# Optimization experiments

Hardware: AMD Instinct MI355X
Metric: run time of the kernel (lower is better)

The kernel has to match this reference:

```python
import jax, jax.numpy as jnp
import numpy as np

B, S, D = 2, 2048, 512
H, DK, DV = 8, 64, 64
TEMP = DK ** 0.5


def setup_inputs() -> dict:
    key = jax.random.key(0)
    ks = jax.random.split(key, 12)
    inp = {
        "q": jax.random.normal(ks[0], (B, S, D), dtype=jnp.float32),
        "k": jax.random.normal(ks[1], (B, S, D), dtype=jnp.float32),
        "v": jax.random.normal(ks[2], (B, S, D), dtype=jnp.float32),
        "static_cov": jax.random.normal(ks[3], (B, S, S), dtype=jnp.float32),
        "mask": jax.random.randint(ks[4], (B, S, S), 0, 2, dtype=jnp.int32),
        # learned params (torch Linear(bias=False) weight is [out,in]; we store [in,out])
        "w_q": jax.random.normal(ks[5], (D, H * DK), dtype=jnp.float32) / np.sqrt(D),
        "w_k": jax.random.normal(ks[6], (D, H * DK), dtype=jnp.float32) / np.sqrt(D),
        "w_v": jax.random.normal(ks[7], (D, H * DV), dtype=jnp.float32) / np.sqrt(D),
        "w_fc": jax.random.normal(ks[8], (H * DV, D), dtype=jnp.float32) / np.sqrt(H * DV),
        "lambda_w": 10.0 * jnp.ones((1, H, 1, 1), dtype=jnp.float32),
        "ln_gamma": jnp.ones((D,), dtype=jnp.float32),
        "ln_beta": jnp.zeros((D,), dtype=jnp.float32),
    }
    return inp


def reference(q, k, v, static_cov, mask, w_q, w_k, w_v, w_fc, lambda_w, ln_gamma, ln_beta):
    residual = q
    # LayerNorm(eps=1e-6) on q only
    mu = jnp.mean(q, axis=-1, keepdims=True)
    var = jnp.mean(jnp.square(q - mu), axis=-1, keepdims=True)
    qn = (q - mu) / jnp.sqrt(var + 1e-6) * ln_gamma + ln_beta
    # projections -> [B, H, S, d]
    qh = (qn @ w_q).reshape(B, S, H, DK).transpose(0, 2, 1, 3)
    kh = (k @ w_k).reshape(B, S, H, DK).transpose(0, 2, 1, 3)
    vh = (v @ w_v).reshape(B, S, H, DV).transpose(0, 2, 1, 3)
    # convex blend of QK^T and static bias
    scores = jnp.einsum('bhqd,bhkd->bhqk', qh / TEMP, kh)  # [B,H,S,S]
    attn = scores / (lambda_w + 1.0) + (lambda_w / (lambda_w + 1.0)) * static_cov[:, None]
    attn = jnp.where(mask[:, None] == 0, -1e9, attn)
    attn = jax.nn.softmax(attn, axis=-1)
    out = jnp.einsum('bhqk,bhkd->bhqd', attn, vh)
    out = out.transpose(0, 2, 1, 3).reshape(B, S, H * DV)
    out = out @ w_fc + residual
    return (out, attn)
```

## Files before the change

kernel.cpp:

```cpp
#include <hip/hip_runtime.h>
#include <hip/hip_bf16.h>

typedef __attribute__((ext_vector_type(4))) float f32x4;
typedef __attribute__((ext_vector_type(4))) int i32x4;
typedef __attribute__((ext_vector_type(4))) unsigned int u32x4;
typedef __attribute__((ext_vector_type(8))) __bf16 bf16x8;
typedef __attribute__((ext_vector_type(4))) __bf16 bf16x4;

#define SDIM 2048
#define DDIM 512
#define HH 8
#define DH 64

static __device__ __forceinline__ f32x4 mfma_raw(bf16x8 a, bf16x8 b, f32x4 c) {
  return __builtin_amdgcn_mfma_f32_16x16x32_bf16(a, b, c, 0, 0, 0);
}

template <bool C1>
static __device__ __forceinline__ f32x4 mf(bf16x8 a, bf16x8 b, f32x4 c) {
  return C1 ? mfma_raw(a, b, c) : mfma_raw(b, a, c);
}

static __device__ __forceinline__ unsigned pack_bf16(float a, float b) {
  __bf16 x = (__bf16)a, y = (__bf16)b;
  unsigned short ux = __builtin_bit_cast(unsigned short, x);
  unsigned short uy = __builtin_bit_cast(unsigned short, y);
  return ((unsigned)uy << 16) | (unsigned)ux;
}

__global__ __launch_bounds__(256) void stageA_kernel(const float* __restrict__ cov,
                                                     const int* __restrict__ mask,
                                                     __bf16* __restrict__ covm,
                                                     const float* __restrict__ q,
                                                     const float* __restrict__ gamma,
                                                     const float* __restrict__ beta,
                                                     __bf16* __restrict__ qn,
                                                     const float* __restrict__ w0,
                                                     const float* __restrict__ w1,
                                                     const float* __restrict__ w2,
                                                     const float* __restrict__ w3,
                                                     __bf16* __restrict__ t0,
                                                     __bf16* __restrict__ t1,
                                                     __bf16* __restrict__ t2,
                                                     __bf16* __restrict__ t3,
                                                     int* __restrict__ flag) {
  __shared__ float tile[64][65];
  int bid = blockIdx.x;
  if (bid < 8192) {
    size_t i = ((size_t)bid * 256 + threadIdx.x) * 4;
    f32x4 c = *(const f32x4*)(cov + i);
    i32x4 m = *(const i32x4*)(mask + i);
    unsigned o = (unsigned)(i & 255);
    unsigned c16 = o >> 4;
    unsigned lgp = (o >> 2) & 3;
    size_t dst = (i & ~(size_t)255) + lgp * 64 + c16 * 4;
    bf16x4 ob;
#pragma unroll
    for (int r = 0; r < 4; ++r) ob[r] = (__bf16)((m[r] == 0) ? -1e38f : c[r]);
    *(bf16x4*)(covm + dst) = ob;
    return;
  }
  if (bid < 9216) {
    int lb = bid - 8192;
    if (lb == 0 && threadIdx.x < 64) {
      float av = (float)(threadIdx.x & 15);
      float bv = av * av;
      bf16x8 a, b;
#pragma unroll
      for (int i = 0; i < 8; ++i) { a[i] = (__bf16)av; b[i] = (__bf16)bv; }
      f32x4 d = {};
      d = mfma_raw(a, b, d);
      if (threadIdx.x == 17) *flag = (d[0] == 128.0f) ? 1 : 2;
    }
    int row = lb * 4 + (threadIdx.x >> 6);
    int lane = threadIdx.x & 63;
    const float* qr = q + (size_t)row * DDIM + lane * 8;
    f32x4 x0 = *(const f32x4*)qr;
    f32x4 x1 = *(const f32x4*)(qr + 4);
    float s = 0.f;
#pragma unroll
    for (int i = 0; i < 4; ++i) s += x0[i] + x1[i];
#pragma unroll
    for (int off = 32; off; off >>= 1) s += __shfl_xor(s, off);
    float mu = s * (1.f / DDIM);
    float vs = 0.f;
#pragma unroll
    for (int i = 0; i < 4; ++i) {
      float d0 = x0[i] - mu, d1 = x1[i] - mu;
      vs += d0 * d0 + d1 * d1;
    }
#pragma unroll
    for (int off = 32; off; off >>= 1) vs += __shfl_xor(vs, off);
    float inv = rsqrtf(vs * (1.f / DDIM) + 1e-6f);
    const float* g = gamma + lane * 8;
    const float* be = beta + lane * 8;
    bf16x8 o;
#pragma unroll
    for (int i = 0; i < 8; ++i) {
      float xv = (i < 4) ? x0[i] : x1[i - 4];
      o[i] = (__bf16)((xv - mu) * inv * g[i] + be[i]);
    }
    *(bf16x8*)(qn + (size_t)row * DDIM + lane * 8) = o;
    return;
  }
  int wb = bid - 9216;
  int which = wb >> 6;
  int rem = wb & 63;
  int n0 = (rem & 7) * 64;
  int k0 = (rem >> 3) * 64;
  const float* w = which == 0 ? w0 : which == 1 ? w1 : which == 2 ? w2 : w3;
  __bf16* t = which == 0 ? t0 : which == 1 ? t1 : which == 2 ? t2 : t3;
  int tx = threadIdx.x & 63, ty = threadIdx.x >> 6;
#pragma unroll
  for (int j = 0; j < 16; ++j) {
    int kk = ty * 16 + j;
    tile[kk][tx] = w[(size_t)(k0 + kk) * DDIM + n0 + tx];
  }
  __syncthreads();
#pragma unroll
  for (int j = 0; j < 16; ++j) {
    int n = ty * 16 + j;
    t[(size_t)(n0 + n) * DDIM + k0 + tx] = (__bf16)tile[tx][n];
  }
}

template <bool C1>
static __device__ __forceinline__ void proj_body(const __bf16* __restrict__ qn,
                                                 const float* __restrict__ kin,
                                                 const float* __restrict__ vin,
                                                 const __bf16* __restrict__ wqT,
                                                 const __bf16* __restrict__ wkT,
                                                 const __bf16* __restrict__ wvT,
                                                 const float* __restrict__ lam,
                                                 __bf16* __restrict__ qh,
                                                 __bf16* __restrict__ kh,
                                                 __bf16* __restrict__ vT,
                                                 __bf16* __restrict__ tr) {
  int which = blockIdx.z;
  int n0 = blockIdx.x * 64;
  int m0 = blockIdx.y * 64;
  int wid = threadIdx.x >> 6, lane = threadIdx.x & 63;
  int lr = lane & 15, lg = lane >> 4;
  int mrow = m0 + wid * 16;
  const __bf16* wT = which == 0 ? wqT : which == 1 ? wkT : wvT;
  f32x4 acc[4] = {};
  for (int kb = 0; kb < DDIM; kb += 32) {
    bf16x8 afrag;
    if (which == 0) {
      afrag = *(const bf16x8*)(qn + (size_t)(mrow + lr) * DDIM + kb + lg * 8);
    } else {
      const float* src = (which == 1 ? kin : vin) + (size_t)(mrow + lr) * DDIM + kb + lg * 8;
      f32x4 y0 = *(const f32x4*)src;
      f32x4 y1 = *(const f32x4*)(src + 4);
#pragma unroll
      for (int i = 0; i < 4; ++i) { afrag[i] = (__bf16)y0[i]; afrag[i + 4] = (__bf16)y1[i]; }
    }
#pragma unroll
    for (int c = 0; c < 4; ++c) {
      bf16x8 bfrag = *(const bf16x8*)(wT + (size_t)(n0 + c * 16 + lr) * DDIM + kb + lg * 8);
      acc[c] = mf<C1>(afrag, bfrag, acc[c]);
    }
  }
  int h = n0 >> 6;
  int bq = m0 >> 11;
  int ss0 = m0 & 2047;
  if (which == 0) {
    float sc = 1.f / (8.f * (lam[h] + 1.f));
#pragma unroll
    for (int c = 0; c < 4; ++c)
#pragma unroll
      for (int r = 0; r < 4; ++r)
        tr[(wid * 16 + lg * 4 + r) * 72 + c * 16 + lr] = (__bf16)(acc[c][r] * sc);
  } else if (which == 1) {
#pragma unroll
    for (int c = 0; c < 4; ++c)
#pragma unroll
      for (int r = 0; r < 4; ++r)
        tr[(wid * 16 + lg * 4 + r) * 72 + c * 16 + lr] = (__bf16)acc[c][r];
  } else {
#pragma unroll
    for (int c = 0; c < 4; ++c)
#pragma unroll
      for (int r = 0; r < 4; ++r)
        tr[(c * 16 + lr) * 72 + wid * 16 + lg * 4 + r] = (__bf16)acc[c][r];
  }
  __syncthreads();
  size_t bh2 = (size_t)bq * HH + h;
#pragma unroll
  for (int ii = 0; ii < 2; ++ii) {
    int row = (threadIdx.x >> 3) + ii * 32;
    int col = (threadIdx.x & 7) * 8;
    bf16x8 v8 = *(const bf16x8*)(tr + row * 72 + col);
    if (which == 2) {
      *(bf16x8*)(vT + (bh2 * DH + row) * SDIM + ss0 + col) = v8;
    } else {
      __bf16* dst = (which == 0 ? qh : kh);
      *(bf16x8*)(dst + (bh2 * SDIM + ss0 + row) * DH + col) = v8;
    }
  }
}

__global__ __launch_bounds__(256) void proj_kernel(const __bf16* __restrict__ qn,
                                                   const float* __restrict__ kin,
                                                   const float* __restrict__ vin,
                                                   const __bf16* __restrict__ wqT,
                                                   const __bf16* __restrict__ wkT,
                                                   const __bf16* __restrict__ wvT,
                                                   const float* __restrict__ lam,
                                                   __bf16* __restrict__ qh,
                                                   __bf16* __restrict__ kh,
                                                   __bf16* __restrict__ vT,
                                                   const int* __restrict__ flag) {
  extern __shared__ __bf16 psm[];
  if (*flag == 1) proj_body<true>(qn, kin, vin, wqT, wkT, wvT, lam, qh, kh, vT, psm);
  else            proj_body<false>(qn, kin, vin, wqT, wkT, wvT, lam, qh, kh, vT, psm);
}

template <bool C1>
static __device__ __forceinline__ void fused_body(const __bf16* __restrict__ qh,
                                                  const __bf16* __restrict__ kh,
                                                  const __bf16* __restrict__ vT,
                                                  const __bf16* __restrict__ covm,
                                                  const float* __restrict__ lam,
                                                  float* __restrict__ attn,
                                                  __bf16* __restrict__ oh,
                                                  float* __restrict__ smem) {
  float* part  = smem;
  float* wredm = smem + 8 * 64 * 17;
  float* wreds = wredm + 128;
  int bid = blockIdx.x;
  int xcd = bid & 7;
  int seq = bid >> 3;
  int bh  = xcd * 2 + (seq & 1);
  int q0  = (seq >> 1) * 16;
  int b = bh >> 3, h = bh & 7;
  int wid = threadIdx.x >> 6, lane = threadIdx.x & 63;
  int lr = lane & 15, lg = lane >> 4;
  int col0 = wid * 256;
  const __bf16* qbase = qh + ((size_t)bh * SDIM + q0) * DH;
  const __bf16* kbase = kh + (size_t)bh * SDIM * DH;
  bf16x8 qf0 = *(const bf16x8*)(qbase + lr * DH + lg * 8);
  bf16x8 qf1 = *(const bf16x8*)(qbase + lr * DH + 32 + lg * 8);
  f32x4 acc[16];
#pragma unroll
  for (int c = 0; c < 16; ++c) {
    const __bf16* kp = kbase + (size_t)(col0 + c * 16 + lr) * DH + lg * 8;
    bf16x8 k0 = *(const bf16x8*)kp;
    bf16x8 k1 = *(const bf16x8*)(kp + 32);
    f32x4 t = {};
    t = mf<C1>(k0, qf0, t);
    t = mf<C1>(k1, qf1, t);
    acc[c] = t;
  }
  float blend = lam[h] / (lam[h] + 1.f);
  const __bf16* crow = covm + ((size_t)b * SDIM + q0 + lr) * SDIM + col0 + lg * 64;
  float mx = -3.4e38f;
#pragma unroll
  for (int cc = 0; cc < 8; ++cc) {
    bf16x8 cv = *(const bf16x8*)(crow + cc * 8);
#pragma unroll
    for (int j = 0; j < 8; ++j) {
      int c = cc * 2 + (j >> 2);
      int r = j & 3;
      float cf = (float)cv[j];
      float valv = acc[c][r] + blend * cf;
      valv = (cf < -1e30f) ? -1e9f : valv;
      acc[c][r] = valv;
      mx = fmaxf(mx, valv);
    }
  }
  mx = fmaxf(mx, __shfl_xor(mx, 16));
  mx = fmaxf(mx, __shfl_xor(mx, 32));
  float sm = 0.f;
#pragma unroll
  for (int c = 0; c < 16; ++c) {
#pragma unroll
    for (int r = 0; r < 4; ++r) {
      float p = __expf(acc[c][r] - mx);
      acc[c][r] = p;
      sm += p;
    }
  }
  sm += __shfl_xor(sm, 16);
  sm += __shfl_xor(sm, 32);
  if (lg == 0) {
    wredm[wid * 16 + lr] = mx;
    wreds[wid * 16 + lr] = sm;
  }
  __syncthreads();
  float M = wredm[lr];
#pragma unroll
  for (int w = 1; w < 8; ++w) M = fmaxf(M, wredm[w * 16 + lr]);
  float denom = 0.f;
#pragma unroll
  for (int w = 0; w < 8; ++w) denom += wreds[w * 16 + lr] * __expf(wredm[w * 16 + lr] - M);
  float sc = __expf(mx - M) / denom;
  const __bf16* vbase = vT + (size_t)bh * DH * SDIM + col0;
  float* abase = attn + ((size_t)bh * SDIM + q0 + lr) * SDIM + col0 + lg * 4;
  int src0 = lr + 32 * (lg & 1);
  int src1 = src0 + 16;
  bool hi = (lg & 2) != 0;
  f32x4 oacc[4] = {};
#pragma unroll
  for (int t = 0; t < 8; ++t) {
    unsigned p0 = pack_bf16(acc[t * 2][0], acc[t * 2][1]);
    unsigned p1 = pack_bf16(acc[t * 2][2], acc[t * 2][3]);
    unsigned p2 = pack_bf16(acc[t * 2 + 1][0], acc[t * 2 + 1][1]);
    unsigned p3 = pack_bf16(acc[t * 2 + 1][2], acc[t * 2 + 1][3]);
    {
      f32x4 pn0, pn1;
#pragma unroll
      for (int r = 0; r < 4; ++r) {
        pn0[r] = acc[t * 2][r] * sc;
        pn1[r] = acc[t * 2 + 1][r] * sc;
      }
      *(f32x4*)(abase + (t * 2) * 16) = pn0;
      *(f32x4*)(abase + (t * 2 + 1) * 16) = pn1;
    }
    unsigned a0 = (unsigned)__shfl((int)p0, src0);
    unsigned a1 = (unsigned)__shfl((int)p1, src0);
    unsigned b0 = (unsigned)__shfl((int)p2, src0);
    unsigned b1 = (unsigned)__shfl((int)p3, src0);
    unsigned a2 = (unsigned)__shfl((int)p0, src1);
    unsigned a3 = (unsigned)__shfl((int)p1, src1);
    unsigned b2 = (unsigned)__shfl((int)p2, src1);
    unsigned b3 = (unsigned)__shfl((int)p3, src1);
    u32x4 wv;
    wv[0] = hi ? b0 : a0;
    wv[1] = hi ? b1 : a1;
    wv[2] = hi ? b2 : a2;
    wv[3] = hi ? b3 : a3;
    bf16x8 pfrag = __builtin_bit_cast(bf16x8, wv);
#pragma unroll
    for (int cp = 0; cp < 4; ++cp) {
      bf16x8 vfrag = *(const bf16x8*)(vbase + (size_t)(cp * 16 + lr) * SDIM + t * 32 + lg * 8);
      oacc[cp] = mf<C1>(vfrag, pfrag, oacc[cp]);
    }
  }
#pragma unroll
  for (int cp = 0; cp < 4; ++cp)
#pragma unroll
    for (int rp = 0; rp < 4; ++rp)
      part[(wid * 64 + cp * 16 + lg * 4 + rp) * 17 + lr] = oacc[cp][rp] * sc;
  __syncthreads();
  {
    int qq = threadIdx.x >> 5;
    int dv = (threadIdx.x & 31) * 2;
    float s0 = 0.f, s1 = 0.f;
#pragma unroll
    for (int w = 0; w < 8; ++w) {
      s0 += part[(w * 64 + dv) * 17 + qq];
      s1 += part[(w * 64 + dv + 1) * 17 + qq];
    }
    unsigned ow = pack_bf16(s0, s1);
    *(unsigned*)(oh + ((size_t)(b * SDIM + q0 + qq)) * DDIM + h * DH + dv) = ow;
  }
}

__global__ __launch_bounds__(512, 4) void fused_kernel_cov(const __bf16* __restrict__ qh,
                                                           const __bf16* __restrict__ kh,
                                                           const __bf16* __restrict__ vT,
                                                           const __bf16* __restrict__ covm,
                                                           const float* __restrict__ lam,
                                                           float* __restrict__ attn,
                                                           __bf16* __restrict__ oh,
                                                           const int* __restrict__ flag) {
  extern __shared__ float smem[];
  if (*flag == 1) fused_body<true>(qh, kh, vT, covm, lam, attn, oh, smem);
  else            fused_body<false>(qh, kh, vT, covm, lam, attn, oh, smem);
}

template <bool C1>
static __device__ __forceinline__ void fc_body(const __bf16* __restrict__ oh,
                                               const __bf16* __restrict__ wfcT,
                                               const float* __restrict__ resid,
                                               float* __restrict__ out) {
  int n0 = blockIdx.x * 64;
  int m0 = blockIdx.y * 64;
  int wid = threadIdx.x >> 6, lane = threadIdx.x & 63;
  int lr = lane & 15, lg = lane >> 4;
  int mrow = m0 + wid * 16;
  f32x4 acc[4] = {};
  for (int kb = 0; kb < DDIM; kb += 32) {
    bf16x8 afrag = *(const bf16x8*)(oh + (size_t)(mrow + lr) * DDIM + kb + lg * 8);
#pragma unroll
    for (int c = 0; c < 4; ++c) {
      bf16x8 bfrag = *(const bf16x8*)(wfcT + (size_t)(n0 + c * 16 + lr) * DDIM + kb + lg * 8);
      acc[c] = mf<C1>(afrag, bfrag, acc[c]);
    }
  }
#pragma unroll
  for (int c = 0; c < 4; ++c)
#pragma unroll
    for (int r = 0; r < 4; ++r) {
      size_t m = mrow + lg * 4 + r;
      size_t n = n0 + c * 16 + lr;
      out[m * DDIM + n] = acc[c][r] + resid[m * DDIM + n];
    }
}

__global__ __launch_bounds__(256) void fc_kernel(const __bf16* __restrict__ oh,
                                                 const __bf16* __restrict__ wfcT,
                                                 const float* __restrict__ resid,
                                                 float* __restrict__ out,
                                                 const int* __restrict__ flag) {
  if (*flag == 1) fc_body<true>(oh, wfcT, resid, out);
  else            fc_body<false>(oh, wfcT, resid, out);
}

extern "C" void kernel_launch(void* const* d_in, const int* in_sizes, int n_in,
                              void* d_out, int out_size, void* d_ws, size_t ws_size,
                              hipStream_t stream) {
  const float* q = (const float*)d_in[0];
  const float* k = (const float*)d_in[1];
  const float* v = (const float*)d_in[2];
  const float* static_cov = (const float*)d_in[3];
  const int* mask = (const int*)d_in[4];
  const float* w_q = (const float*)d_in[5];
  const float* w_k = (const float*)d_in[6];
  const float* w_v = (const float*)d_in[7];
  const float* w_fc = (const float*)d_in[8];
  const float* lam = (const float*)d_in[9];
  const float* gamma = (const float*)d_in[10];
  const float* beta = (const float*)d_in[11];

  float* out = (float*)d_out;
  float* attn = out + (size_t)2 * SDIM * DDIM;

  char* ws = (char*)d_ws;
  const size_t MB4 = (size_t)4 << 20;
  __bf16* qn  = (__bf16*)(ws);
  __bf16* qh  = (__bf16*)(ws + 1 * MB4);
  __bf16* kh  = (__bf16*)(ws + 2 * MB4);
  __bf16* vT  = (__bf16*)(ws + 3 * MB4);
  __bf16* oh  = (__bf16*)(ws + 4 * MB4);
  __bf16* wqT = (__bf16*)(ws + 5 * MB4);
  __bf16* wkT = (__bf16*)(ws + 5 * MB4 + 524288);
  __bf16* wvT = (__bf16*)(ws + 5 * MB4 + 2 * 524288);
  __bf16* wfcT= (__bf16*)(ws + 5 * MB4 + 3 * 524288);
  int* flag   = (int*)(ws + 5 * MB4 + 4 * 524288);
  __bf16* covm = (__bf16*)(ws + 6 * MB4);

  const unsigned fused_smem = (8 * 64 * 17 + 128 + 128) * 4;
  const unsigned proj_smem  = 64 * 72 * 2;

  stageA_kernel<<<dim3(9472), dim3(256), 0, stream>>>(static_cov, mask, covm,
                                                      q, gamma, beta, qn,
                                                      w_q, w_k, w_v, w_fc,
                                                      wqT, wkT, wvT, wfcT, flag);
  proj_kernel<<<dim3(8, 64, 3), dim3(256), proj_smem, stream>>>(qn, k, v, wqT, wkT, wvT, lam, qh, kh, vT, flag);
  fused_kernel_cov<<<dim3(2048), dim3(512), fused_smem, stream>>>(qh, kh, vT, covm, lam, attn, oh, flag);
  fc_kernel<<<dim3(8, 64), dim3(256), 0, stream>>>(oh, wfcT, q, out, flag);
}
```

Measured before the change: 272.0 us.

## Keep projection A-fragments in registers and loop over heads per block

Each projection block now loads its 64-row activation slice once into registers (16 bf16x8 fragments) and loops over all 8 heads, rather than one block per head re-reading and re-converting the same fp32 K/V rows. This removes the 8x redundant activation loads and conversions. The cost is that the grid shrinks from 1536 to 192 blocks, which is below one block per CU on a large GPU. Register pressure also rises, and an extra barrier is added per head iteration.

```diff
diff --git a/kernel.cpp b/kernel.cpp
--- a/kernel.cpp
+++ b/kernel.cpp
@@ -136,81 +136,92 @@
                                                  __bf16* __restrict__ kh,
                                                  __bf16* __restrict__ vT,
                                                  __bf16* __restrict__ tr) {
-  int which = blockIdx.z;
-  int n0 = blockIdx.x * 64;
-  int m0 = blockIdx.y * 64;
+  int which = blockIdx.y;
+  int m0 = blockIdx.x * 64;
   int wid = threadIdx.x >> 6, lane = threadIdx.x & 63;
   int lr = lane & 15, lg = lane >> 4;
   int mrow = m0 + wid * 16;
   const __bf16* wT = which == 0 ? wqT : which == 1 ? wkT : wvT;
-  f32x4 acc[4] = {};
-  for (int kb = 0; kb < DDIM; kb += 32) {
-    bf16x8 afrag;
-    if (which == 0) {
-      afrag = *(const bf16x8*)(qn + (size_t)(mrow + lr) * DDIM + kb + lg * 8);
-    } else {
-      const float* src = (which == 1 ? kin : vin) + (size_t)(mrow + lr) * DDIM + kb + lg * 8;
+  bf16x8 af[16];
+  if (which == 0) {
+#pragma unroll
+    for (int kb = 0; kb < 16; ++kb)
+      af[kb] = *(const bf16x8*)(qn + (size_t)(mrow + lr) * DDIM + kb * 32 + lg * 8);
+  } else {
+    const float* A = which == 1 ? kin : vin;
+#pragma unroll
+    for (int kb = 0; kb < 16; ++kb) {
+      const float* src = A + (size_t)(mrow + lr) * DDIM + kb * 32 + lg * 8;
       f32x4 y0 = *(const f32x4*)src;
       f32x4 y1 = *(const f32x4*)(src + 4);
-#pragma unroll
-      for (int i = 0; i < 4; ++i) { afrag[i] = (__bf16)y0[i]; afrag[i + 4] = (__bf16)y1[i]; }
-    }
-#pragma unroll
-    for (int c = 0; c < 4; ++c) {
-      bf16x8 bfrag = *(const bf16x8*)(wT + (size_t)(n0 + c * 16 + lr) * DDIM + kb + lg * 8);
-      acc[c] = mf<C1>(afrag, bfrag, acc[c]);
-    }
-  }
-  int h = n0 >> 6;
+      bf16x8 a;
+#pragma unroll
+      for (int i = 0; i < 4; ++i) { a[i] = (__bf16)y0[i]; a[i + 4] = (__bf16)y1[i]; }
+      af[kb] = a;
+    }
+  }
   int bq = m0 >> 11;
   int ss0 = m0 & 2047;
-  if (which == 0) {
-    float sc = 1.f / (8.f * (lam[h] + 1.f));
-#pragma unroll
-    for (int c = 0; c < 4; ++c)
-#pragma unroll
-      for (int r = 0; r < 4; ++r)
-        tr[(wid * 16 + lg * 4 + r) * 72 + c * 16 + lr] = (__bf16)(acc[c][r] * sc);
-  } else if (which == 1) {
-#pragma unroll
-    for (int c = 0; c < 4; ++c)
-#pragma unroll
-      for (int r = 0; r < 4; ++r)
-        tr[(wid * 16 + lg * 4 + r) * 72 + c * 16 + lr] = (__bf16)acc[c][r];
-  } else {
-#pragma unroll
-    for (int c = 0; c < 4; ++c)
-#pragma unroll
-      for (int r = 0; r < 4; ++r)
-        tr[(c * 16 + lr) * 72 + wid * 16 + lg * 4 + r] = (__bf16)acc[c][r];
-  }
-  __syncthreads();
-  size_t bh2 = (size_t)bq * HH + h;
-#pragma unroll
-  for (int ii = 0; ii < 2; ++ii) {
-    int row = (threadIdx.x >> 3) + ii * 32;
-    int col = (threadIdx.x & 7) * 8;
-    bf16x8 v8 = *(const bf16x8*)(tr + row * 72 + col);
-    if (which == 2) {
-      *(bf16x8*)(vT + (bh2 * DH + row) * SDIM + ss0 + col) = v8;
+  for (int h = 0; h < 8; ++h) {
+    int n0 = h * 64;
+    f32x4 acc[4] = {};
+#pragma unroll
+    for (int kb = 0; kb < 16; ++kb) {
+#pragma unroll
+      for (int c = 0; c < 4; ++c) {
+        bf16x8 bfrag = *(const bf16x8*)(wT + (size_t)(n0 + c * 16 + lr) * DDIM + kb * 32 + lg * 8);
+        acc[c] = mf<C1>(af[kb], bfrag, acc[c]);
+      }
+    }
+    if (which == 0) {
+      float sc = 1.f / (8.f * (lam[h] + 1.f));
+#pragma unroll
+      for (int c = 0; c < 4; ++c)
+#pragma unroll
+        for (int r = 0; r < 4; ++r)
+          tr[(wid * 16 + lg * 4 + r) * 72 + c * 16 + lr] = (__bf16)(acc[c][r] * sc);
+    } else if (which == 1) {
+#pragma unroll
+      for (int c = 0; c < 4; ++c)
+#pragma unroll
+        for (int r = 0; r < 4; ++r)
+          tr[(wid * 16 + lg * 4 + r) * 72 + c * 16 + lr] = (__bf16)acc[c][r];
     } else {
-      __bf16* dst = (which == 0 ? qh : kh);
-      *(bf16x8*)(dst + (bh2 * SDIM + ss0 + row) * DH + col) = v8;
-    }
-  }
-}
-
-__global__ __launch_bounds__(256) void proj_kernel(const __bf16* __restrict__ qn,
-                                                   const float* __restrict__ kin,
-                                                   const float* __restrict__ vin,
-                                                   const __bf16* __restrict__ wqT,
-                                                   const __bf16* __restrict__ wkT,
-                                                   const __bf16* __restrict__ wvT,
-                                                   const float* __restrict__ lam,
-                                                   __bf16* __restrict__ qh,
-                                                   __bf16* __restrict__ kh,
-                                                   __bf16* __restrict__ vT,
-                                                   const int* __restrict__ flag) {
+#pragma unroll
+      for (int c = 0; c < 4; ++c)
+#pragma unroll
+        for (int r = 0; r < 4; ++r)
+          tr[(c * 16 + lr) * 72 + wid * 16 + lg * 4 + r] = (__bf16)acc[c][r];
+    }
+    __syncthreads();
+    size_t bh2 = (size_t)bq * HH + h;
+#pragma unroll
+    for (int ii = 0; ii < 2; ++ii) {
+      int row = (threadIdx.x >> 3) + ii * 32;
+      int col = (threadIdx.x & 7) * 8;
+      bf16x8 v8 = *(const bf16x8*)(tr + row * 72 + col);
+      if (which == 2) {
+        *(bf16x8*)(vT + (bh2 * DH + row) * SDIM + ss0 + col) = v8;
+      } else {
+        __bf16* dst = (which == 0 ? qh : kh);
+        *(bf16x8*)(dst + (bh2 * SDIM + ss0 + row) * DH + col) = v8;
+      }
+    }
+    __syncthreads();
+  }
+}
+
+__global__ __launch_bounds__(256, 2) void proj_kernel(const __bf16* __restrict__ qn,
+                                                      const float* __restrict__ kin,
+                                                      const float* __restrict__ vin,
+                                                      const __bf16* __restrict__ wqT,
+                                                      const __bf16* __restrict__ wkT,
+                                                      const __bf16* __restrict__ wvT,
+                                                      const float* __restrict__ lam,
+                                                      __bf16* __restrict__ qh,
+                                                      __bf16* __restrict__ kh,
+                                                      __bf16* __restrict__ vT,
+                                                      const int* __restrict__ flag) {
   extern __shared__ __bf16 psm[];
   if (*flag == 1) proj_body<true>(qn, kin, vin, wqT, wkT, wvT, lam, qh, kh, vT, psm);
   else            proj_body<false>(qn, kin, vin, wqT, wkT, wvT, lam, qh, kh, vT, psm);
@@ -448,7 +459,7 @@
                                                       q, gamma, beta, qn,
                                                       w_q, w_k, w_v, w_fc,
                                                       wqT, wkT, wvT, wfcT, flag);
-  proj_kernel<<<dim3(8, 64, 3), dim3(256), proj_smem, stream>>>(qn, k, v, wqT, wkT, wvT, lam, qh, kh, vT, flag);
+  proj_kernel<<<dim3(64, 3), dim3(256), proj_smem, stream>>>(qn, k, v, wqT, wkT, wvT, lam, qh, kh, vT, flag);
   fused_kernel_cov<<<dim3(2048), dim3(512), fused_smem, stream>>>(qh, kh, vT, covm, lam, attn, oh, flag);
   fc_kernel<<<dim3(8, 64), dim3(256), 0, stream>>>(oh, wfcT, q, out, flag);
 }
```

Measured after the change: 281.6 us. 1.04x slower.
